# Optimization experiments

Hardware: AMD Instinct MI355X
Metric: run time of the kernel (lower is better)

Reference implementation:

```python
import jax, jax.numpy as jnp
import numpy as np

BN_EPS = 1e-5

def _mlp(x, W1, b1, g1, beta1, W2, b2):
    # Linear -> BatchNorm1d (training-mode batch stats) -> ReLU -> Linear
    z = x @ W1 + b1
    mu = z.mean(axis=0)
    var = z.var(axis=0)  # biased, matching torch BN normalization
    z = (z - mu) * jax.lax.rsqrt(var + BN_EPS) * g1 + beta1
    z = jax.nn.relu(z)
    return z @ W2 + b2

def setup_inputs() -> dict:
    key = jax.random.key(0)
    ks = jax.random.split(key, 32)
    N, E, G, D = 100000, 500000, 5000, 128
    H = 3 * D  # hidden size = out_size*3
    inp = {
        'h': jax.random.normal(ks[0], (N, D), jnp.float32),
        'e': jax.random.normal(ks[1], (E, D), jnp.float32),
        'u': jax.random.normal(ks[2], (G, D), jnp.float32),
        'src': jax.random.randint(ks[3], (E,), 0, N, jnp.int32),
        'dst': jax.random.randint(ks[4], (E,), 0, N, jnp.int32),
        'graph_id': jnp.sort(jax.random.randint(ks[5], (N,), 0, G, jnp.int32)),
    }
    # three MLPs, all with input 3*D=384, hidden 384, output D=128
    names = ['b', 'a', 'g']  # bond, atom, global
    for i, n in enumerate(names):
        k0, k1 = ks[6 + 2 * i], ks[7 + 2 * i]
        inp[n + 'W1'] = jax.random.normal(k0, (3 * D, H), jnp.float32) * 0.05
        inp[n + 'b1'] = jnp.zeros((H,), jnp.float32)
        inp[n + 'g1'] = jnp.ones((H,), jnp.float32)
        inp[n + 'beta1'] = jnp.zeros((H,), jnp.float32)
        inp[n + 'W2'] = jax.random.normal(k1, (H, D), jnp.float32) * 0.05
        inp[n + 'b2'] = jnp.zeros((D,), jnp.float32)
    return inp

def reference(h, e, u, src, dst, graph_id,
              bW1, bb1, bg1, bbeta1, bW2, bb2,
              aW1, ab1, ag1, abeta1, aW2, ab2,
              gW1, gb1, gg1, gbeta1, gW2, gb2):
    N = h.shape[0]
    G = u.shape[0]
    # g2a: copy_u + sum with a single global per atom == gather
    u_node = u[graph_id]            # [N, D]
    u_edge = u_node[src]            # [E, D]
    # bond update: cat(h_src + h_dst, e, u_edge) -> mlp_bond
    sum_h_edge = h[src] + h[dst]
    e_new = _mlp(jnp.concatenate([sum_h_edge, e, u_edge], axis=-1),
                 bW1, bb1, bg1, bbeta1, bW2, bb2)
    # atom update: scatter-sum of updated bond feats and neighbor h onto dst
    sum_e = jax.ops.segment_sum(e_new, dst, num_segments=N)
    sum_h = jax.ops.segment_sum(h[src], dst, num_segments=N) + h
    h_new = _mlp(jnp.concatenate([sum_h, sum_e, u_node], axis=-1),
                 aW1, ab1, ag1, abeta1, aW2, ab2)
    # global update: a2g segment sums per molecule
    sum_e_g = 0.5 * jax.ops.segment_sum(sum_e, graph_id, num_segments=G)
    sum_h_g = jax.ops.segment_sum(h_new, graph_id, num_segments=G)
    u_new = _mlp(jnp.concatenate([sum_h_g, sum_e_g, u], axis=-1),
                 gW1, gb1, gg1, gbeta1, gW2, gb2)
    return h_new, e_new, u_new
```

## Files before the change

kernel.cpp:

```cpp
#include <hip/hip_runtime.h>
#include <hip/hip_bf16.h>
#include <stdint.h>

#define D 128
#define KTOT 384
#define BN_EPS 1e-5f

typedef __attribute__((ext_vector_type(8))) short short8;
typedef __attribute__((ext_vector_type(4))) float floatx4;

__device__ __forceinline__ unsigned short f2bf(float f) {
    __hip_bfloat16 b = __float2bfloat16(f);
    return *reinterpret_cast<unsigned short*>(&b);
}
__device__ __forceinline__ float bf2f(unsigned short u) {
    unsigned int b = ((unsigned int)u) << 16;
    return __uint_as_float(b);
}

__global__ void convert_transpose_kernel(const float* __restrict__ W,
                                         unsigned short* __restrict__ WT,
                                         int K, int N)
{
    int idx = blockIdx.x * 256 + threadIdx.x;
    if (idx >= K * N) return;
    int k = idx / N, n = idx % N;
    WT[(size_t)n * K + k] = f2bf(W[idx]);
}

__global__ void hist_kernel(const int* __restrict__ dst, int* __restrict__ deg, int E)
{
    int e = blockIdx.x * 256 + threadIdx.x;
    if (e < E) atomicAdd(&deg[dst[e]], 1);
}

__global__ void scan_block_kernel(const int* __restrict__ deg,
                                  int* __restrict__ offs,
                                  int* __restrict__ bsum, int N)
{
    __shared__ int s[256];
    int i = blockIdx.x * 256 + threadIdx.x;
    int v = (i < N) ? deg[i] : 0;
    s[threadIdx.x] = v;
    __syncthreads();
#pragma unroll
    for (int off = 1; off < 256; off <<= 1) {
        int t = (threadIdx.x >= off) ? s[threadIdx.x - off] : 0;
        __syncthreads();
        s[threadIdx.x] += t;
        __syncthreads();
    }
    if (i < N) offs[i] = s[threadIdx.x] - v;
    if (threadIdx.x == 255) bsum[blockIdx.x] = s[255];
}

__global__ void scan_bsum_kernel(int* __restrict__ bsum, int B)
{
    __shared__ int s[512];
    int i = threadIdx.x;
    int v = (i < B) ? bsum[i] : 0;
    s[i] = v;
    __syncthreads();
#pragma unroll
    for (int off = 1; off < 512; off <<= 1) {
        int t = (i >= off) ? s[i - off] : 0;
        __syncthreads();
        s[i] += t;
        __syncthreads();
    }
    if (i < B) bsum[i] = s[i] - v;
}

__global__ void scan_add_cursor_kernel(int* __restrict__ offs,
                                       const int* __restrict__ bsum,
                                       int* __restrict__ cursor, int N)
{
    int i = blockIdx.x * 256 + threadIdx.x;
    if (i < N) {
        int o = offs[i] + bsum[blockIdx.x];
        offs[i] = o;
        cursor[i] = o;
    }
}

__global__ void fill_kernel(const int* __restrict__ src,
                            const int* __restrict__ dst,
                            int* __restrict__ cursor,
                            int* __restrict__ el_src,
                            int* __restrict__ el_e, int E)
{
    int e = blockIdx.x * 256 + threadIdx.x;
    if (e < E) {
        int p = atomicAdd(&cursor[dst[e]], 1);
        el_src[p] = src[e];
        el_e[p] = e;
    }
}

__global__ void gather_sum_h_kernel(const float* __restrict__ h,
                                    const int* __restrict__ offs,
                                    const int* __restrict__ el_src,
                                    float* __restrict__ sum_h, int N, int E)
{
    int t = blockIdx.x * 256 + threadIdx.x;
    int n = t >> 5;
    if (n >= N) return;
    int c = (t & 31) * 4;
    float4 acc = *(const float4*)(h + (size_t)n * D + c);
    int p = offs[n];
    int pe = (n + 1 < N) ? offs[n + 1] : E;
    for (; p < pe; ++p) {
        int s = el_src[p];
        const float4 v = *(const float4*)(h + (size_t)s * D + c);
        acc.x += v.x; acc.y += v.y; acc.z += v.z; acc.w += v.w;
    }
    *(float4*)(sum_h + (size_t)n * D + c) = acc;
}

__global__ void gather_sum_e_kernel(const float* __restrict__ e_new,
                                    const int* __restrict__ offs,
                                    const int* __restrict__ el_e,
                                    float* __restrict__ sum_e, int N, int E)
{
    int t = blockIdx.x * 256 + threadIdx.x;
    int n = t >> 5;
    if (n >= N) return;
    int c = (t & 31) * 4;
    float4 acc = {0.f, 0.f, 0.f, 0.f};
    int p = offs[n];
    int pe = (n + 1 < N) ? offs[n + 1] : E;
    for (; p < pe; ++p) {
        int e = el_e[p];
        const float4 v = *(const float4*)(e_new + (size_t)e * D + c);
        acc.x += v.x; acc.y += v.y; acc.z += v.z; acc.w += v.w;
    }
    *(float4*)(sum_e + (size_t)n * D + c) = acc;
}

__global__ __launch_bounds__(128)
void graph_seg_sum_kernel(const float* __restrict__ h_new,
                          const float* __restrict__ sum_e,
                          const int* __restrict__ gid,
                          float* __restrict__ sum_hg,
                          float* __restrict__ sum_eg, int N)
{
    int g = blockIdx.x;
    int lo = 0, hi = N;
    while (lo < hi) { int m = (lo + hi) >> 1; if (gid[m] < g) lo = m + 1; else hi = m; }
    int s0 = lo;
    hi = N;
    while (lo < hi) { int m = (lo + hi) >> 1; if (gid[m] < g + 1) lo = m + 1; else hi = m; }
    int e0 = lo;
    int c = threadIdx.x;
    float aH = 0.f, aE = 0.f;
    for (int n = s0; n < e0; ++n) {
        aH += h_new[(size_t)n * D + c];
        aE += sum_e[(size_t)n * D + c];
    }
    sum_hg[(size_t)g * D + c] = aH;
    sum_eg[(size_t)g * D + c] = 0.5f * aE;
}

template<int MODE>
__global__ __launch_bounds__(256)
void gemm1_mfma_kernel(const float* __restrict__ P0,
                       const float* __restrict__ P1,
                       const float* __restrict__ P2,
                       const int* __restrict__ src,
                       const int* __restrict__ dst,
                       const int* __restrict__ graph_id,
                       const unsigned short* __restrict__ W1T,
                       const float* __restrict__ b1,
                       unsigned short* __restrict__ z,
                       float* __restrict__ stat_sum,
                       float* __restrict__ stat_sq,
                       int M)
{
    __shared__ __align__(16) char smem[37376];
    short (*As)[40] = (short(*)[40])smem;
    short (*Bs)[40] = (short(*)[40])(smem + 10240);
    short (*Zs)[136] = (short(*)[136])smem;
    int* s_i0 = (int*)(smem + 34816);
    int* s_i1 = s_i0 + 128;
    int* s_i2 = s_i1 + 128;
    float* s_sum = (float*)(smem + 36352);
    float* s_sq  = s_sum + 128;

    const int tid = threadIdx.x;
    const int row0 = blockIdx.x * 128;
    const int colblk = blockIdx.y * 128;

    if (tid < 128) {
        int r = row0 + tid;
        bool v = r < M;
        if (MODE == 0) {
            int s = v ? src[r] : 0;
            int d = v ? dst[r] : 0;
            s_i0[tid] = s; s_i1[tid] = d;
            s_i2[tid] = v ? graph_id[s] : 0;
        } else if (MODE == 1) {
            s_i2[tid] = v ? graph_id[r] : 0;
        }
        s_sum[tid] = 0.f; s_sq[tid] = 0.f;
    }
    __syncthreads();

    const int lane = tid & 63;
    const int wave = tid >> 6;
    const int wm = wave >> 1, wn = wave & 1;
    const int txl = lane & 15;
    const int quad = lane >> 4;
    const int kofs = quad * 8;

    const int r2 = tid >> 1;
    const int khalf = (tid & 1) * 16;

    floatx4 acc[4][4] = {};

    for (int kt = 0; kt < KTOT; kt += 32) {
        {
            int gk = kt + khalf;
            float v[16];
            int grow = row0 + r2;
            if (grow < M) {
                const float4* q0; const float4* q1 = nullptr;
                if (MODE == 0) {
                    if (gk < 128) {
                        q0 = (const float4*)(P0 + (size_t)s_i0[r2] * D + gk);
                        q1 = (const float4*)(P0 + (size_t)s_i1[r2] * D + gk);
                    } else if (gk < 256) {
                        q0 = (const float4*)(P1 + (size_t)grow * D + (gk - 128));
                    } else {
                        q0 = (const float4*)(P2 + (size_t)s_i2[r2] * D + (gk - 256));
                    }
                } else if (MODE == 1) {
                    if (gk < 128)      q0 = (const float4*)(P0 + (size_t)grow * D + gk);
                    else if (gk < 256) q0 = (const float4*)(P1 + (size_t)grow * D + (gk - 128));
                    else               q0 = (const float4*)(P2 + (size_t)s_i2[r2] * D + (gk - 256));
                } else {
                    if (gk < 128)      q0 = (const float4*)(P0 + (size_t)grow * D + gk);
                    else if (gk < 256) q0 = (const float4*)(P1 + (size_t)grow * D + (gk - 128));
                    else               q0 = (const float4*)(P2 + (size_t)grow * D + (gk - 256));
                }
#pragma unroll
                for (int q = 0; q < 4; q++) {
                    float4 a = q0[q];
                    if (MODE == 0 && q1) {
                        float4 b = q1[q];
                        a.x += b.x; a.y += b.y; a.z += b.z; a.w += b.w;
                    }
                    v[q * 4 + 0] = a.x; v[q * 4 + 1] = a.y;
                    v[q * 4 + 2] = a.z; v[q * 4 + 3] = a.w;
                }
            } else {
#pragma unroll
                for (int m = 0; m < 16; m++) v[m] = 0.f;
            }
            unsigned short t16[16];
#pragma unroll
            for (int m = 0; m < 16; m++) t16[m] = f2bf(v[m]);
            uint4* dp = (uint4*)&As[r2][khalf];
            dp[0] = *(const uint4*)&t16[0];
            dp[1] = *(const uint4*)&t16[8];
        }
        {
            const uint4* gp = (const uint4*)(W1T + (size_t)(colblk + r2) * KTOT + kt + khalf);
            uint4* dp = (uint4*)&Bs[r2][khalf];
            dp[0] = gp[0];
            dp[1] = gp[1];
        }
        __syncthreads();

        short8 af[4], bfr[4];
#pragma unroll
        for (int i = 0; i < 4; i++) af[i]  = *(const short8*)&As[wm * 64 + i * 16 + txl][kofs];
#pragma unroll
        for (int j = 0; j < 4; j++) bfr[j] = *(const short8*)&Bs[wn * 64 + j * 16 + txl][kofs];
#pragma unroll
        for (int i = 0; i < 4; i++)
#pragma unroll
            for (int j = 0; j < 4; j++)
                acc[i][j] = __builtin_amdgcn_mfma_f32_16x16x32_bf16(af[i], bfr[j], acc[i][j], 0, 0, 0);
        __syncthreads();
    }

    float bias[4];
#pragma unroll
    for (int j = 0; j < 4; j++) bias[j] = b1[colblk + wn * 64 + j * 16 + txl];
    float csum[4] = {0.f, 0.f, 0.f, 0.f}, csq[4] = {0.f, 0.f, 0.f, 0.f};
#pragma unroll
    for (int i = 0; i < 4; i++) {
        int rl = wm * 64 + i * 16 + quad * 4;
#pragma unroll
        for (int j = 0; j < 4; j++) {
            int cl = wn * 64 + j * 16 + txl;
            floatx4 a = acc[i][j];
#pragma unroll
            for (int reg = 0; reg < 4; reg++) {
                float zv = a[reg] + bias[j];
                Zs[rl + reg][cl] = (short)f2bf(zv);
                if (row0 + rl + reg < M) { csum[j] += zv; csq[j] += zv * zv; }
            }
        }
    }
#pragma unroll
    for (int j = 0; j < 4; j++) {
        atomicAdd(&s_sum[wn * 64 + j * 16 + txl], csum[j]);
        atomicAdd(&s_sq[wn * 64 + j * 16 + txl], csq[j]);
    }
    __syncthreads();

    {
        int grow = row0 + r2;
        if (grow < M) {
            const short* srcp = &Zs[r2][(tid & 1) * 64];
            unsigned short* dstp = z + (size_t)grow * KTOT + colblk + (tid & 1) * 64;
#pragma unroll
            for (int q = 0; q < 8; q++) {
                *(uint4*)(dstp + q * 8) = *(const uint4*)(srcp + q * 8);
            }
        }
    }
    if (tid < 128) {
        atomicAdd(&stat_sum[colblk + tid], s_sum[tid]);
        atomicAdd(&stat_sq[colblk + tid], s_sq[tid]);
    }
}

__global__ void bn_finalize_kernel(const float* __restrict__ ssum,
                                   const float* __restrict__ ssq,
                                   const float* __restrict__ g1,
                                   const float* __restrict__ beta1,
                                   float invM,
                                   float* __restrict__ scale,
                                   float* __restrict__ shift)
{
    int j = threadIdx.x;
    if (j < KTOT) {
        float mu = ssum[j] * invM;
        float var = ssq[j] * invM - mu * mu;
        float sc = g1[j] * rsqrtf(var + BN_EPS);
        scale[j] = sc;
        shift[j] = beta1[j] - mu * sc;
    }
}

__global__ __launch_bounds__(256)
void gemm2_mfma_kernel(const unsigned short* __restrict__ z,
                       const float* __restrict__ scale,
                       const float* __restrict__ shift,
                       const unsigned short* __restrict__ W2T,
                       const float* __restrict__ b2,
                       float* __restrict__ out,
                       int M)
{
    __shared__ __align__(16) short As[128][40];
    __shared__ __align__(16) short Bs[128][40];
    __shared__ float s_scale[KTOT], s_shift[KTOT];

    const int tid = threadIdx.x;
    const int row0 = blockIdx.x * 128;

    for (int i = tid; i < KTOT; i += 256) { s_scale[i] = scale[i]; s_shift[i] = shift[i]; }
    __syncthreads();

    const int lane = tid & 63;
    const int wave = tid >> 6;
    const int wm = wave >> 1, wn = wave & 1;
    const int txl = lane & 15;
    const int quad = lane >> 4;
    const int kofs = quad * 8;

    const int r2 = tid >> 1;
    const int khalf = (tid & 1) * 16;

    floatx4 acc[4][4] = {};

    for (int kt = 0; kt < KTOT; kt += 32) {
        {
            int gk = kt + khalf;
            int grow = row0 + r2;
            unsigned short t16[16];
            if (grow < M) {
                const uint4* gp = (const uint4*)(z + (size_t)grow * KTOT + gk);
                uint4 w0 = gp[0], w1 = gp[1];
                const unsigned short* us = (const unsigned short*)&w0;
#pragma unroll
                for (int m = 0; m < 8; m++) {
                    float f = bf2f(us[m]);
                    f = fmaxf(f * s_scale[gk + m] + s_shift[gk + m], 0.f);
                    t16[m] = f2bf(f);
                }
                const unsigned short* us1 = (const unsigned short*)&w1;
#pragma unroll
                for (int m = 0; m < 8; m++) {
                    float f = bf2f(us1[m]);
                    f = fmaxf(f * s_scale[gk + 8 + m] + s_shift[gk + 8 + m], 0.f);
                    t16[8 + m] = f2bf(f);
                }
            } else {
#pragma unroll
                for (int m = 0; m < 16; m++) t16[m] = 0;
            }
            uint4* dp = (uint4*)&As[r2][khalf];
            dp[0] = *(const uint4*)&t16[0];
            dp[1] = *(const uint4*)&t16[8];
        }
        {
            const uint4* gp = (const uint4*)(W2T + (size_t)r2 * KTOT + kt + khalf);
            uint4* dp = (uint4*)&Bs[r2][khalf];
            dp[0] = gp[0];
            dp[1] = gp[1];
        }
        __syncthreads();

        short8 af[4], bfr[4];
#pragma unroll
        for (int i = 0; i < 4; i++) af[i]  = *(const short8*)&As[wm * 64 + i * 16 + txl][kofs];
#pragma unroll
        for (int j = 0; j < 4; j++) bfr[j] = *(const short8*)&Bs[wn * 64 + j * 16 + txl][kofs];
#pragma unroll
        for (int i = 0; i < 4; i++)
#pragma unroll
            for (int j = 0; j < 4; j++)
                acc[i][j] = __builtin_amdgcn_mfma_f32_16x16x32_bf16(af[i], bfr[j], acc[i][j], 0, 0, 0);
        __syncthreads();
    }

    float bias[4];
#pragma unroll
    for (int j = 0; j < 4; j++) bias[j] = b2[wn * 64 + j * 16 + txl];
#pragma unroll
    for (int i = 0; i < 4; i++) {
#pragma unroll
        for (int reg = 0; reg < 4; reg++) {
            int rl = wm * 64 + i * 16 + quad * 4 + reg;
            int grow = row0 + rl;
            if (grow < M) {
#pragma unroll
                for (int j = 0; j < 4; j++) {
                    int c = wn * 64 + j * 16 + txl;
                    out[(size_t)grow * D + c] = acc[i][j][reg] + bias[j];
                }
            }
        }
    }
}

extern "C" void kernel_launch(void* const* d_in, const int* in_sizes, int n_in,
                              void* d_out, int out_size, void* d_ws, size_t ws_size,
                              hipStream_t stream)
{
    const float* h  = (const float*)d_in[0];
    const float* e  = (const float*)d_in[1];
    const float* u  = (const float*)d_in[2];
    const int* src  = (const int*)d_in[3];
    const int* dst  = (const int*)d_in[4];
    const int* gid  = (const int*)d_in[5];

    const float* bW1 = (const float*)d_in[6];  const float* bb1 = (const float*)d_in[7];
    const float* bg1 = (const float*)d_in[8];  const float* bbe = (const float*)d_in[9];
    const float* bW2 = (const float*)d_in[10]; const float* bb2 = (const float*)d_in[11];
    const float* aW1 = (const float*)d_in[12]; const float* ab1 = (const float*)d_in[13];
    const float* ag1 = (const float*)d_in[14]; const float* abe = (const float*)d_in[15];
    const float* aW2 = (const float*)d_in[16]; const float* ab2 = (const float*)d_in[17];
    const float* gW1 = (const float*)d_in[18]; const float* gb1 = (const float*)d_in[19];
    const float* gg1 = (const float*)d_in[20]; const float* gbe = (const float*)d_in[21];
    const float* gW2 = (const float*)d_in[22]; const float* gb2 = (const float*)d_in[23];

    const int N = in_sizes[0] / D;
    const int E = in_sizes[1] / D;
    const int G = in_sizes[2] / D;

    float* out   = (float*)d_out;
    float* h_new = out;
    float* e_new = out + (size_t)N * D;
    float* u_new = out + (size_t)N * D + (size_t)E * D;

    char* ws = (char*)d_ws;
    unsigned short* z = (unsigned short*)ws;
    size_t off = ((size_t)E * KTOT * sizeof(unsigned short) + 255) & ~(size_t)255;
    float* sum_e  = (float*)(ws + off); off += ((size_t)N * D * 4 + 255) & ~(size_t)255;
    float* sum_h  = (float*)(ws + off); off += ((size_t)N * D * 4 + 255) & ~(size_t)255;
    float* sum_hg = (float*)(ws + off); off += ((size_t)G * D * 4 + 255) & ~(size_t)255;
    float* sum_eg = (float*)(ws + off); off += ((size_t)G * D * 4 + 255) & ~(size_t)255;
    float* st_sum = (float*)(ws + off); off += KTOT * 4;
    float* st_sq  = (float*)(ws + off); off += KTOT * 4;
    float* bn_sc  = (float*)(ws + off); off += KTOT * 4;
    float* bn_sh  = (float*)(ws + off); off += KTOT * 4;
    off = (off + 255) & ~(size_t)255;
    unsigned short* w1t_b = (unsigned short*)(ws + off); off += (size_t)KTOT * KTOT * 2;
    unsigned short* w2t_b = (unsigned short*)(ws + off); off += (size_t)KTOT * D * 2;
    unsigned short* w1t_a = (unsigned short*)(ws + off); off += (size_t)KTOT * KTOT * 2;
    unsigned short* w2t_a = (unsigned short*)(ws + off); off += (size_t)KTOT * D * 2;
    unsigned short* w1t_g = (unsigned short*)(ws + off); off += (size_t)KTOT * KTOT * 2;
    unsigned short* w2t_g = (unsigned short*)(ws + off); off += (size_t)KTOT * D * 2;
    off = (off + 255) & ~(size_t)255;
    int* deg     = (int*)(ws + off); off += ((size_t)N * 4 + 255) & ~(size_t)255;
    int* offs    = (int*)(ws + off); off += ((size_t)N * 4 + 255) & ~(size_t)255;
    int* cursor  = (int*)(ws + off); off += ((size_t)N * 4 + 255) & ~(size_t)255;
    int* bsum    = (int*)(ws + off); off += ((size_t)1024 * 4 + 255) & ~(size_t)255;
    int* el_src  = (int*)(ws + off); off += ((size_t)E * 4 + 255) & ~(size_t)255;
    int* el_e    = (int*)(ws + off); off += ((size_t)E * 4 + 255) & ~(size_t)255;

    const dim3 blk(256);
    const int NB = (N + 255) / 256;

    {
        int n1 = KTOT * KTOT, n2 = KTOT * D;
        convert_transpose_kernel<<<(n1 + 255) / 256, blk, 0, stream>>>(bW1, w1t_b, KTOT, KTOT);
        convert_transpose_kernel<<<(n2 + 255) / 256, blk, 0, stream>>>(bW2, w2t_b, KTOT, D);
        convert_transpose_kernel<<<(n1 + 255) / 256, blk, 0, stream>>>(aW1, w1t_a, KTOT, KTOT);
        convert_transpose_kernel<<<(n2 + 255) / 256, blk, 0, stream>>>(aW2, w2t_a, KTOT, D);
        convert_transpose_kernel<<<(n1 + 255) / 256, blk, 0, stream>>>(gW1, w1t_g, KTOT, KTOT);
        convert_transpose_kernel<<<(n2 + 255) / 256, blk, 0, stream>>>(gW2, w2t_g, KTOT, D);
    }

    hipMemsetAsync(deg, 0, (size_t)N * 4, stream);
    hist_kernel<<<(E + 255) / 256, blk, 0, stream>>>(dst, deg, E);
    scan_block_kernel<<<NB, blk, 0, stream>>>(deg, offs, bsum, N);
    scan_bsum_kernel<<<1, 512, 0, stream>>>(bsum, NB);
    scan_add_cursor_kernel<<<NB, blk, 0, stream>>>(offs, bsum, cursor, N);
    fill_kernel<<<(E + 255) / 256, blk, 0, stream>>>(src, dst, cursor, el_src, el_e, E);

    gather_sum_h_kernel<<<(N * 32 + 255) / 256, blk, 0, stream>>>(h, offs, el_src, sum_h, N, E);

    hipMemsetAsync(st_sum, 0, KTOT * 4, stream);
    hipMemsetAsync(st_sq,  0, KTOT * 4, stream);
    gemm1_mfma_kernel<0><<<dim3((E + 127) / 128, 3), blk, 0, stream>>>(
        h, e, u, src, dst, gid, w1t_b, bb1, z, st_sum, st_sq, E);
    bn_finalize_kernel<<<1, KTOT, 0, stream>>>(st_sum, st_sq, bg1, bbe, 1.0f / (float)E, bn_sc, bn_sh);
    gemm2_mfma_kernel<<<dim3((E + 127) / 128, 1), blk, 0, stream>>>(
        z, bn_sc, bn_sh, w2t_b, bb2, e_new, E);

    gather_sum_e_kernel<<<(N * 32 + 255) / 256, blk, 0, stream>>>(e_new, offs, el_e, sum_e, N, E);

    hipMemsetAsync(st_sum, 0, KTOT * 4, stream);
    hipMemsetAsync(st_sq,  0, KTOT * 4, stream);
    gemm1_mfma_kernel<1><<<dim3((N + 127) / 128, 3), blk, 0, stream>>>(
        sum_h, sum_e, u, src, dst, gid, w1t_a, ab1, z, st_sum, st_sq, N);
    bn_finalize_kernel<<<1, KTOT, 0, stream>>>(st_sum, st_sq, ag1, abe, 1.0f / (float)N, bn_sc, bn_sh);
    gemm2_mfma_kernel<<<dim3((N + 127) / 128, 1), blk, 0, stream>>>(
        z, bn_sc, bn_sh, w2t_a, ab2, h_new, N);

    graph_seg_sum_kernel<<<G, 128, 0, stream>>>(h_new, sum_e, gid, sum_hg, sum_eg, N);

    hipMemsetAsync(st_sum, 0, KTOT * 4, stream);
    hipMemsetAsync(st_sq,  0, KTOT * 4, stream);
    gemm1_mfma_kernel<2><<<dim3((G + 127) / 128, 3), blk, 0, stream>>>(
        sum_hg, sum_eg, u, src, dst, gid, w1t_g, gb1, z, st_sum, st_sq, G);
    bn_finalize_kernel<<<1, KTOT, 0, stream>>>(st_sum, st_sq, gg1, gbe, 1.0f / (float)G, bn_sc, bn_sh);
    gemm2_mfma_kernel<<<dim3((G + 127) / 128, 1), blk, 0, stream>>>(
        z, bn_sc, bn_sh, w2t_g, gb2, u_new, G);
}
```

Measured before the change: 1.696 ms.

## Compute all hidden columns per block in gemm1 to avoid repeated gathers

gemm1 now has each block compute all 384 output columns of its 128-row tile rather than splitting columns across a 3-wide grid dimension. The gathered/summed A operand (indexed node rows, edge features, global features) is loaded and converted to bf16 once instead of three times. The B tile, accumulators and BN stat buffers grow to cover all columns, and the epilogue writes the three column chunks sequentially through shared memory. This trades larger register and shared-memory use, with lower occupancy and possible spilling, for removing redundant irregular global reads.

```diff
diff --git a/kernel.cpp b/kernel.cpp
--- a/kernel.cpp
+++ b/kernel.cpp
@@ -162,7 +162,7 @@
 }
 
 template<int MODE>
-__global__ __launch_bounds__(256)
+__global__ __launch_bounds__(256, 2)
 void gemm1_mfma_kernel(const float* __restrict__ P0,
                        const float* __restrict__ P1,
                        const float* __restrict__ P2,
@@ -176,19 +176,18 @@
                        float* __restrict__ stat_sq,
                        int M)
 {
-    __shared__ __align__(16) char smem[37376];
+    __shared__ __align__(16) char smem[45568];
     short (*As)[40] = (short(*)[40])smem;
     short (*Bs)[40] = (short(*)[40])(smem + 10240);
     short (*Zs)[136] = (short(*)[136])smem;
-    int* s_i0 = (int*)(smem + 34816);
+    int* s_i0 = (int*)(smem + 40960);
     int* s_i1 = s_i0 + 128;
     int* s_i2 = s_i1 + 128;
-    float* s_sum = (float*)(smem + 36352);
-    float* s_sq  = s_sum + 128;
+    float* s_sum = (float*)(smem + 42496);
+    float* s_sq  = s_sum + 384;
 
     const int tid = threadIdx.x;
     const int row0 = blockIdx.x * 128;
-    const int colblk = blockIdx.y * 128;
 
     if (tid < 128) {
         int r = row0 + tid;
@@ -201,8 +200,8 @@
         } else if (MODE == 1) {
             s_i2[tid] = v ? graph_id[r] : 0;
         }
-        s_sum[tid] = 0.f; s_sq[tid] = 0.f;
-    }
+    }
+    for (int i = tid; i < KTOT; i += 256) { s_sum[i] = 0.f; s_sq[i] = 0.f; }
     __syncthreads();
 
     const int lane = tid & 63;
@@ -215,13 +214,13 @@
     const int r2 = tid >> 1;
     const int khalf = (tid & 1) * 16;
 
-    floatx4 acc[4][4] = {};
+    floatx4 acc[4][12] = {};
 
     for (int kt = 0; kt < KTOT; kt += 32) {
         {
             int gk = kt + khalf;
-            float v[16];
             int grow = row0 + r2;
+            unsigned short t16[16];
             if (grow < M) {
                 const float4* q0; const float4* q1 = nullptr;
                 if (MODE == 0) {
@@ -249,68 +248,75 @@
                         float4 b = q1[q];
                         a.x += b.x; a.y += b.y; a.z += b.z; a.w += b.w;
                     }
-                    v[q * 4 + 0] = a.x; v[q * 4 + 1] = a.y;
-                    v[q * 4 + 2] = a.z; v[q * 4 + 3] = a.w;
+                    t16[q * 4 + 0] = f2bf(a.x); t16[q * 4 + 1] = f2bf(a.y);
+                    t16[q * 4 + 2] = f2bf(a.z); t16[q * 4 + 3] = f2bf(a.w);
                 }
             } else {
 #pragma unroll
-                for (int m = 0; m < 16; m++) v[m] = 0.f;
+                for (int m = 0; m < 16; m++) t16[m] = 0;
             }
-            unsigned short t16[16];
-#pragma unroll
-            for (int m = 0; m < 16; m++) t16[m] = f2bf(v[m]);
             uint4* dp = (uint4*)&As[r2][khalf];
             dp[0] = *(const uint4*)&t16[0];
             dp[1] = *(const uint4*)&t16[8];
         }
-        {
-            const uint4* gp = (const uint4*)(W1T + (size_t)(colblk + r2) * KTOT + kt + khalf);
-            uint4* dp = (uint4*)&Bs[r2][khalf];
+#pragma unroll
+        for (int c = 0; c < 3; c++) {
+            const uint4* gp = (const uint4*)(W1T + (size_t)(c * 128 + r2) * KTOT + kt + khalf);
+            uint4* dp = (uint4*)&Bs[c * 128 + r2][khalf];
             dp[0] = gp[0];
             dp[1] = gp[1];
         }
         __syncthreads();
 
-        short8 af[4], bfr[4];
-#pragma unroll
-        for (int i = 0; i < 4; i++) af[i]  = *(const short8*)&As[wm * 64 + i * 16 + txl][kofs];
-#pragma unroll
-        for (int j = 0; j < 4; j++) bfr[j] = *(const short8*)&Bs[wn * 64 + j * 16 + txl][kofs];
-#pragma unroll
-        for (int i = 0; i < 4; i++)
+        short8 af[4];
+#pragma unroll
+        for (int i = 0; i < 4; i++) af[i] = *(const short8*)&As[wm * 64 + i * 16 + txl][kofs];
+#pragma unroll
+        for (int c = 0; c < 3; c++) {
+            short8 bfr[4];
 #pragma unroll
             for (int j = 0; j < 4; j++)
-                acc[i][j] = __builtin_amdgcn_mfma_f32_16x16x32_bf16(af[i], bfr[j], acc[i][j], 0, 0, 0);
-        __syncthreads();
-    }
-
-    float bias[4];
-#pragma unroll
-    for (int j = 0; j < 4; j++) bias[j] = b1[colblk + wn * 64 + j * 16 + txl];
-    float csum[4] = {0.f, 0.f, 0.f, 0.f}, csq[4] = {0.f, 0.f, 0.f, 0.f};
-#pragma unroll
-    for (int i = 0; i < 4; i++) {
-        int rl = wm * 64 + i * 16 + quad * 4;
+                bfr[j] = *(const short8*)&Bs[c * 128 + wn * 64 + j * 16 + txl][kofs];
+#pragma unroll
+            for (int i = 0; i < 4; i++)
+#pragma unroll
+                for (int j = 0; j < 4; j++)
+                    acc[i][c * 4 + j] = __builtin_amdgcn_mfma_f32_16x16x32_bf16(
+                        af[i], bfr[j], acc[i][c * 4 + j], 0, 0, 0);
+        }
+        __syncthreads();
+    }
+
+#pragma unroll
+    for (int c = 0; c < 3; c++) {
+        const int colblk = c * 128;
+        float bias[4];
+#pragma unroll
+        for (int j = 0; j < 4; j++) bias[j] = b1[colblk + wn * 64 + j * 16 + txl];
+        if (c > 0) __syncthreads();
+        float csum[4] = {0.f, 0.f, 0.f, 0.f}, csq[4] = {0.f, 0.f, 0.f, 0.f};
+#pragma unroll
+        for (int i = 0; i < 4; i++) {
+            int rl = wm * 64 + i * 16 + quad * 4;
+#pragma unroll
+            for (int j = 0; j < 4; j++) {
+                int cl = wn * 64 + j * 16 + txl;
+                floatx4 a = acc[i][c * 4 + j];
+#pragma unroll
+                for (int reg = 0; reg < 4; reg++) {
+                    float zv = a[reg] + bias[j];
+                    Zs[rl + reg][cl] = (short)f2bf(zv);
+                    if (row0 + rl + reg < M) { csum[j] += zv; csq[j] += zv * zv; }
+                }
+            }
+        }
 #pragma unroll
         for (int j = 0; j < 4; j++) {
-            int cl = wn * 64 + j * 16 + txl;
-            floatx4 a = acc[i][j];
-#pragma unroll
-            for (int reg = 0; reg < 4; reg++) {
-                float zv = a[reg] + bias[j];
-                Zs[rl + reg][cl] = (short)f2bf(zv);
-                if (row0 + rl + reg < M) { csum[j] += zv; csq[j] += zv * zv; }
-            }
-        }
-    }
-#pragma unroll
-    for (int j = 0; j < 4; j++) {
-        atomicAdd(&s_sum[wn * 64 + j * 16 + txl], csum[j]);
-        atomicAdd(&s_sq[wn * 64 + j * 16 + txl], csq[j]);
-    }
-    __syncthreads();
-
-    {
+            atomicAdd(&s_sum[colblk + wn * 64 + j * 16 + txl], csum[j]);
+            atomicAdd(&s_sq[colblk + wn * 64 + j * 16 + txl], csq[j]);
+        }
+        __syncthreads();
+
         int grow = row0 + r2;
         if (grow < M) {
             const short* srcp = &Zs[r2][(tid & 1) * 64];
@@ -321,9 +327,9 @@
             }
         }
     }
-    if (tid < 128) {
-        atomicAdd(&stat_sum[colblk + tid], s_sum[tid]);
-        atomicAdd(&stat_sq[colblk + tid], s_sq[tid]);
+    for (int i = tid; i < KTOT; i += 256) {
+        atomicAdd(&stat_sum[i], s_sum[i]);
+        atomicAdd(&stat_sq[i], s_sq[i]);
     }
 }
 
@@ -527,29 +533,29 @@
 
     hipMemsetAsync(st_sum, 0, KTOT * 4, stream);
     hipMemsetAsync(st_sq,  0, KTOT * 4, stream);
-    gemm1_mfma_kernel<0><<<dim3((E + 127) / 128, 3), blk, 0, stream>>>(
+    gemm1_mfma_kernel<0><<<dim3((E + 127) / 128), blk, 0, stream>>>(
         h, e, u, src, dst, gid, w1t_b, bb1, z, st_sum, st_sq, E);
     bn_finalize_kernel<<<1, KTOT, 0, stream>>>(st_sum, st_sq, bg1, bbe, 1.0f / (float)E, bn_sc, bn_sh);
-    gemm2_mfma_kernel<<<dim3((E + 127) / 128, 1), blk, 0, stream>>>(
+    gemm2_mfma_kernel<<<dim3((E + 127) / 128), blk, 0, stream>>>(
         z, bn_sc, bn_sh, w2t_b, bb2, e_new, E);
 
     gather_sum_e_kernel<<<(N * 32 + 255) / 256, blk, 0, stream>>>(e_new, offs, el_e, sum_e, N, E);
 
     hipMemsetAsync(st_sum, 0, KTOT * 4, stream);
     hipMemsetAsync(st_sq,  0, KTOT * 4, stream);
-    gemm1_mfma_kernel<1><<<dim3((N + 127) / 128, 3), blk, 0, stream>>>(
+    gemm1_mfma_kernel<1><<<dim3((N + 127) / 128), blk, 0, stream>>>(
         sum_h, sum_e, u, src, dst, gid, w1t_a, ab1, z, st_sum, st_sq, N);
     bn_finalize_kernel<<<1, KTOT, 0, stream>>>(st_sum, st_sq, ag1, abe, 1.0f / (float)N, bn_sc, bn_sh);
-    gemm2_mfma_kernel<<<dim3((N + 127) / 128, 1), blk, 0, stream>>>(
+    gemm2_mfma_kernel<<<dim3((N + 127) / 128), blk, 0, stream>>>(
         z, bn_sc, bn_sh, w2t_a, ab2, h_new, N);
 
     graph_seg_sum_kernel<<<G, 128, 0, stream>>>(h_new, sum_e, gid, sum_hg, sum_eg, N);
 
     hipMemsetAsync(st_sum, 0, KTOT * 4, stream);
     hipMemsetAsync(st_sq,  0, KTOT * 4, stream);
-    gemm1_mfma_kernel<2><<<dim3((G + 127) / 128, 3), blk, 0, stream>>>(
+    gemm1_mfma_kernel<2><<<dim3((G + 127) / 128), blk, 0, stream>>>(
         sum_hg, sum_eg, u, src, dst, gid, w1t_g, gb1, z, st_sum, st_sq, G);
     bn_finalize_kernel<<<1, KTOT, 0, stream>>>(st_sum, st_sq, gg1, gbe, 1.0f / (float)G, bn_sc, bn_sh);
-    gemm2_mfma_kernel<<<dim3((G + 127) / 128, 1), blk, 0, stream>>>(
+    gemm2_mfma_kernel<<<dim3((G + 127) / 128), blk, 0, stream>>>(
         z, bn_sc, bn_sh, w2t_g, gb2, u_new, G);
 }
```

New measurement: 1.851 ms. 9.2% more time.
